# Performance work log

Measured on AMD Instinct MI355X. Metric: run time of the kernel, lower is better.

The kernel has to match this reference:

```python
import jax, jax.numpy as jnp
import numpy as np

EPSILON = 0.1
ALPHA = 0.5
N_ITER = 10
N_USERS = 100000


def setup_inputs() -> dict:
    key = jax.random.key(0)
    k1, k2, k3, k4, k5, k6 = jax.random.split(key, 6)
    B, C, F = 2048, 1024, 128
    users = jax.random.randint(k1, (B,), 0, N_USERS)
    items = jax.random.randint(k2, (B, C), 0, C)
    D = jax.random.uniform(k3, (B, C), minval=0.1, maxval=1.0)
    capacities = jax.random.uniform(k4, (C,), minval=0.5, maxval=1.5)
    # ScaledEmbedding: normal init scaled down by embedding_dim
    item_emb = jax.random.normal(k5, (C, F), dtype=jnp.float32) / F
    user_emb = jax.random.normal(k6, (N_USERS, F), dtype=jnp.float32) / F
    return dict(users=users, items=items, D=D, capacities=capacities,
                item_emb=item_emb, user_emb=user_emb)


def reference(users, items, D, capacities, item_emb, user_emb):
    B, C = D.shape
    ie = item_emb[items]            # [B, C, F] gathered candidate embeddings
    ue = user_emb[users]            # [B, F]
    dot = jnp.einsum('bcf,bf->bc', ie, ue)          # batched dot products
    affinity = (1.0 - ALPHA) * dot - ALPHA * (D / jnp.mean(D))
    K = jnp.exp(affinity / EPSILON)                 # [B, C]

    scaling = B / N_USERS
    a = jnp.ones((B,), K.dtype)
    b = capacities * scaling                        # [C]

    def step(carry, _):
        _, v = carry
        u = a / (K @ v)                             # [B]
        v_new = b / (K.T @ u)                       # [C]
        return (u, v_new), None

    (u, v), _ = jax.lax.scan(step, (a, jnp.ones((C,), K.dtype)),
                             None, length=N_ITER)
    P = K * (u[:, None] * v[None, :])               # K * outer(u, v)
    return P
```

## Files before the change

kernel.cpp:

```cpp
#include <hip/hip_runtime.h>
#include <hip/hip_fp16.h>

#define BB      2048
#define CC      1024
#define FF      128
#define NBLK    256
#define RPB     8
#define TPB     512
#define NITER   10
#define SUBR    8
#define SCALING_F (2048.0f / 100000.0f)

__device__ float g_K[BB * CC];
__device__ float g_meanPart[NBLK];
__device__ float g_colsum[NITER * SUBR * CC];

__global__ void __launch_bounds__(TPB)
k0_prep(const float* __restrict__ D) {
    const int bid = blockIdx.x, tid = threadIdx.x;
    for (int i = bid * TPB + tid; i < NITER * SUBR * CC; i += NBLK * TPB)
        g_colsum[i] = 0.0f;
    const float4* D4 = (const float4*)D;
    float p = 0.0f;
    for (int i = bid * TPB + tid; i < BB * CC / 4; i += NBLK * TPB) {
        float4 d = D4[i];
        p += d.x + d.y + d.z + d.w;
    }
    #pragma unroll
    for (int off = 32; off > 0; off >>= 1) p += __shfl_down(p, off, 64);
    __shared__ float red[TPB / 64];
    if ((tid & 63) == 0) red[tid >> 6] = p;
    __syncthreads();
    if (tid == 0) {
        float s = 0.0f;
        #pragma unroll
        for (int k = 0; k < TPB / 64; ++k) s += red[k];
        g_meanPart[bid] = s;
    }
}

__global__ void __launch_bounds__(TPB)
k1_buildK(const int* __restrict__ users, const int* __restrict__ items,
          const float* __restrict__ D, const float* __restrict__ iemb,
          const float* __restrict__ uemb) {
    const int bid = blockIdx.x, tid = threadIdx.x;
    const int r0 = bid * RPB;

    __shared__ float  uesh[RPB][FF];
    __shared__ __half dott[RPB][CC];
    __shared__ float  s2sh;

    if (tid < 256) {
        int r = tid >> 5, f4 = tid & 31;
        int u = users[r0 + r];
        ((float4*)uesh[r])[f4] = ((const float4*)(uemb + (size_t)u * FF))[f4];
    }
    if (tid < 64) {
        float s = g_meanPart[tid] + g_meanPart[tid + 64] +
                  g_meanPart[tid + 128] + g_meanPart[tid + 192];
        #pragma unroll
        for (int off = 32; off > 0; off >>= 1) s += __shfl_down(s, off, 64);
        if (tid == 0) s2sh = 5.0f * (float)(BB * CC) / s;
    }
    __syncthreads();

    const float4* us = (const float4*)uesh;
    #pragma unroll
    for (int jj = 0; jj < CC / TPB; ++jj) {
        int j = jj * TPB + tid;
        float acc[RPB] = {};
        const float4* ip = (const float4*)(iemb + (size_t)j * FF);
        for (int f4 = 0; f4 < FF / 4; ++f4) {
            float4 a = ip[f4];
            #pragma unroll
            for (int r = 0; r < RPB; ++r) {
                float4 b = us[r * (FF / 4) + f4];
                acc[r] += a.x * b.x + a.y * b.y + a.z * b.z + a.w * b.w;
            }
        }
        #pragma unroll
        for (int r = 0; r < RPB; ++r) dott[r][j] = __float2half(acc[r]);
    }
    __syncthreads();

    const float s2 = s2sh;
    const int4*   it4 = (const int4*)(items + ((size_t)r0 << 10));
    const float4* D4  = (const float4*)(D + ((size_t)r0 << 10));
    float4*       K4  = (float4*)(g_K + ((size_t)r0 << 10));
    for (int i = tid; i < RPB * CC / 4; i += TPB) {
        int4 iv = it4[i];
        float4 d = D4[i];
        int r = i >> 8;
        float4 kv;
        kv.x = __expf(5.0f * __half2float(dott[r][iv.x]) - s2 * d.x);
        kv.y = __expf(5.0f * __half2float(dott[r][iv.y]) - s2 * d.y);
        kv.z = __expf(5.0f * __half2float(dott[r][iv.z]) - s2 * d.z);
        kv.w = __expf(5.0f * __half2float(dott[r][iv.w]) - s2 * d.w);
        K4[i] = kv;
    }
}

__global__ void __launch_bounds__(TPB)
k_iter(const float* __restrict__ caps, int t) {
    const int bid = blockIdx.x, tid = threadIdx.x;
    const int r0 = bid * RPB;

    __shared__ float Kt[RPB][CC];
    __shared__ float vsh[CC];
    __shared__ float ush[RPB];

    for (int c = tid; c < CC; c += TPB) {
        float v = 1.0f;
        if (t > 0) {
            const float* base = g_colsum + (size_t)(t - 1) * SUBR * CC;
            float s = 0.0f;
            #pragma unroll
            for (int k = 0; k < SUBR; ++k) s += base[k * CC + c];
            v = caps[c] * SCALING_F / s;
        }
        vsh[c] = v;
    }
    const float4* Kg = (const float4*)(g_K + ((size_t)r0 << 10));
    float4* KtL = (float4*)Kt;
    for (int i = tid; i < RPB * CC / 4; i += TPB) KtL[i] = Kg[i];
    __syncthreads();

    {
        int r = tid >> 6, l = tid & 63;
        const float4* kr = (const float4*)Kt[r];
        const float4* v4 = (const float4*)vsh;
        float p = 0.0f;
        #pragma unroll
        for (int i = 0; i < 4; ++i) {
            float4 k = kr[l + i * 64], v = v4[l + i * 64];
            p += k.x * v.x + k.y * v.y + k.z * v.z + k.w * v.w;
        }
        #pragma unroll
        for (int off = 32; off > 0; off >>= 1) p += __shfl_down(p, off, 64);
        if (l == 0) ush[r] = 1.0f / p;
    }
    __syncthreads();

    float* cb = g_colsum + ((size_t)t * SUBR + (bid & (SUBR - 1))) * CC;
    for (int c = tid; c < CC; c += TPB) {
        float s = 0.0f;
        #pragma unroll
        for (int r = 0; r < RPB; ++r) s += Kt[r][c] * ush[r];
        atomicAdd(&cb[c], s);
    }
}

__global__ void __launch_bounds__(TPB)
k_final(const float* __restrict__ caps, float* __restrict__ out) {
    const int bid = blockIdx.x, tid = threadIdx.x;
    const int r0 = bid * RPB;

    __shared__ float Kt[RPB][CC];
    __shared__ float vsh[CC];
    __shared__ float ush[RPB];

    for (int c = tid; c < CC; c += TPB) {
        const float* base = g_colsum + (size_t)(NITER - 2) * SUBR * CC;
        float s = 0.0f;
        #pragma unroll
        for (int k = 0; k < SUBR; ++k) s += base[k * CC + c];
        vsh[c] = caps[c] * SCALING_F / s;
    }
    const float4* Kg = (const float4*)(g_K + ((size_t)r0 << 10));
    float4* KtL = (float4*)Kt;
    for (int i = tid; i < RPB * CC / 4; i += TPB) KtL[i] = Kg[i];
    __syncthreads();

    {
        int r = tid >> 6, l = tid & 63;
        const float4* kr = (const float4*)Kt[r];
        const float4* v4 = (const float4*)vsh;
        float p = 0.0f;
        #pragma unroll
        for (int i = 0; i < 4; ++i) {
            float4 k = kr[l + i * 64], v = v4[l + i * 64];
            p += k.x * v.x + k.y * v.y + k.z * v.z + k.w * v.w;
        }
        #pragma unroll
        for (int off = 32; off > 0; off >>= 1) p += __shfl_down(p, off, 64);
        if (l == 0) ush[r] = 1.0f / p;
    }
    __syncthreads();

    for (int c = tid; c < CC; c += TPB) {
        const float* base = g_colsum + (size_t)(NITER - 1) * SUBR * CC;
        float s = 0.0f;
        #pragma unroll
        for (int k = 0; k < SUBR; ++k) s += base[k * CC + c];
        vsh[c] = caps[c] * SCALING_F / s;
    }
    __syncthreads();

    float4* o4 = (float4*)(out + ((size_t)r0 << 10));
    for (int i = tid; i < RPB * CC / 4; i += TPB) {
        int r = i >> 8;
        float4 k = KtL[i];
        float  ur = ush[r];
        float4 v = *(const float4*)&vsh[(i * 4) & (CC - 1)];
        float4 p;
        p.x = k.x * ur * v.x;  p.y = k.y * ur * v.y;
        p.z = k.z * ur * v.z;  p.w = k.w * ur * v.w;
        o4[i] = p;
    }
}

extern "C" void kernel_launch(void* const* d_in, const int* in_sizes, int n_in,
                              void* d_out, int out_size, void* d_ws, size_t ws_size,
                              hipStream_t stream) {
    const int*   users = (const int*)d_in[0];
    const int*   items = (const int*)d_in[1];
    const float* D     = (const float*)d_in[2];
    const float* caps  = (const float*)d_in[3];
    const float* iemb  = (const float*)d_in[4];
    const float* uemb  = (const float*)d_in[5];
    float* out = (float*)d_out;

    hipLaunchKernelGGL(k0_prep,   dim3(NBLK), dim3(TPB), 0, stream, D);
    hipLaunchKernelGGL(k1_buildK, dim3(NBLK), dim3(TPB), 0, stream,
                       users, items, D, iemb, uemb);
    for (int t = 0; t < NITER; ++t)
        hipLaunchKernelGGL(k_iter, dim3(NBLK), dim3(TPB), 0, stream, caps, t);
    hipLaunchKernelGGL(k_final,  dim3(NBLK), dim3(TPB), 0, stream, caps, out);
}
```

Baseline: 192.6 us.

## Fuse all Sinkhorn stages into one cooperative persistent kernel with grid syncs

Replaces the thirteen separate launches (prep, K build, ten iterations, final) with one cooperative kernel that uses grid-wide syncs between phases. Each block keeps its 8-row K tile resident in shared memory for the whole run, so the global K buffer and its per-iteration reloads go away, and D is read only once. The costs removed are launch gaps and repeated 8 MB K traffic. In exchange the kernel depends on all 256 blocks being co-resident, uses more shared memory per block, and pays a grid barrier on every iteration.

```diff
diff --git a/kernel.cpp b/kernel.cpp
--- a/kernel.cpp
+++ b/kernel.cpp
@@ -1,5 +1,8 @@
 #include <hip/hip_runtime.h>
 #include <hip/hip_fp16.h>
+#include <hip/hip_cooperative_groups.h>
+
+namespace cg = cooperative_groups;
 
 #define BB      2048
 #define CC      1024
@@ -11,60 +14,55 @@
 #define SUBR    8
 #define SCALING_F (2048.0f / 100000.0f)
 
-__device__ float g_K[BB * CC];
 __device__ float g_meanPart[NBLK];
 __device__ float g_colsum[NITER * SUBR * CC];
 
 __global__ void __launch_bounds__(TPB)
-k0_prep(const float* __restrict__ D) {
+fused_sinkhorn(const int* __restrict__ users, const int* __restrict__ items,
+               const float* __restrict__ D, const float* __restrict__ caps,
+               const float* __restrict__ iemb, const float* __restrict__ uemb,
+               float* __restrict__ out) {
     const int bid = blockIdx.x, tid = threadIdx.x;
+    const int r0 = bid * RPB;
+
+    __shared__ union { float ue[RPB][FF]; float v[CC]; } uv;
+    __shared__ __half dott[RPB][CC];
+    __shared__ float  Kt[RPB][CC];
+    __shared__ float  ush[RPB];
+    __shared__ float  red[TPB / 64];
+    __shared__ float  s2sh;
+
     for (int i = bid * TPB + tid; i < NITER * SUBR * CC; i += NBLK * TPB)
-        g_colsum[i] = 0.0f;
-    const float4* D4 = (const float4*)D;
+        __hip_atomic_store(&g_colsum[i], 0.0f, __ATOMIC_RELAXED,
+                           __HIP_MEMORY_SCOPE_AGENT);
+
+    if (tid < 256) {
+        int r = tid >> 5, f4 = tid & 31;
+        int u = users[r0 + r];
+        ((float4*)uv.ue[r])[f4] = ((const float4*)(uemb + (size_t)u * FF))[f4];
+    }
+
+    const float4* Dg  = (const float4*)(D + ((size_t)r0 << 10));
+    float4*       KtL = (float4*)Kt;
     float p = 0.0f;
-    for (int i = bid * TPB + tid; i < BB * CC / 4; i += NBLK * TPB) {
-        float4 d = D4[i];
+    for (int i = tid; i < RPB * CC / 4; i += TPB) {
+        float4 d = Dg[i];
+        KtL[i] = d;
         p += d.x + d.y + d.z + d.w;
     }
     #pragma unroll
     for (int off = 32; off > 0; off >>= 1) p += __shfl_down(p, off, 64);
-    __shared__ float red[TPB / 64];
     if ((tid & 63) == 0) red[tid >> 6] = p;
     __syncthreads();
     if (tid == 0) {
         float s = 0.0f;
         #pragma unroll
         for (int k = 0; k < TPB / 64; ++k) s += red[k];
-        g_meanPart[bid] = s;
+        __hip_atomic_store(&g_meanPart[bid], s, __ATOMIC_RELAXED,
+                           __HIP_MEMORY_SCOPE_AGENT);
     }
-}
 
-__global__ void __launch_bounds__(TPB)
-k1_buildK(const int* __restrict__ users, const int* __restrict__ items,
-          const float* __restrict__ D, const float* __restrict__ iemb,
-          const float* __restrict__ uemb) {
-    const int bid = blockIdx.x, tid = threadIdx.x;
-    const int r0 = bid * RPB;
-
-    __shared__ float  uesh[RPB][FF];
-    __shared__ __half dott[RPB][CC];
-    __shared__ float  s2sh;
-
-    if (tid < 256) {
-        int r = tid >> 5, f4 = tid & 31;
-        int u = users[r0 + r];
-        ((float4*)uesh[r])[f4] = ((const float4*)(uemb + (size_t)u * FF))[f4];
-    }
-    if (tid < 64) {
-        float s = g_meanPart[tid] + g_meanPart[tid + 64] +
-                  g_meanPart[tid + 128] + g_meanPart[tid + 192];
-        #pragma unroll
-        for (int off = 32; off > 0; off >>= 1) s += __shfl_down(s, off, 64);
-        if (tid == 0) s2sh = 5.0f * (float)(BB * CC) / s;
-    }
-    __syncthreads();
-
-    const float4* us = (const float4*)uesh;
+    const float4* us = (const float4*)uv.ue;
     #pragma unroll
     for (int jj = 0; jj < CC / TPB; ++jj) {
         int j = jj * TPB + tid;
@@ -81,131 +79,100 @@
         #pragma unroll
         for (int r = 0; r < RPB; ++r) dott[r][j] = __float2half(acc[r]);
     }
+
+    cg::this_grid().sync();
+
+    if (tid < 64) {
+        float s = 0.0f;
+        #pragma unroll
+        for (int k = 0; k < NBLK / 64; ++k)
+            s += __hip_atomic_load(&g_meanPart[tid + 64 * k], __ATOMIC_RELAXED,
+                                   __HIP_MEMORY_SCOPE_AGENT);
+        #pragma unroll
+        for (int off = 32; off > 0; off >>= 1) s += __shfl_down(s, off, 64);
+        if (tid == 0) s2sh = 5.0f * (float)(BB * CC) / s;
+    }
     __syncthreads();
-
     const float s2 = s2sh;
-    const int4*   it4 = (const int4*)(items + ((size_t)r0 << 10));
-    const float4* D4  = (const float4*)(D + ((size_t)r0 << 10));
-    float4*       K4  = (float4*)(g_K + ((size_t)r0 << 10));
+    const int4* it4 = (const int4*)(items + ((size_t)r0 << 10));
     for (int i = tid; i < RPB * CC / 4; i += TPB) {
-        int4 iv = it4[i];
-        float4 d = D4[i];
-        int r = i >> 8;
+        int4   iv = it4[i];
+        float4 d  = KtL[i];
+        int    r  = i >> 8;
         float4 kv;
         kv.x = __expf(5.0f * __half2float(dott[r][iv.x]) - s2 * d.x);
         kv.y = __expf(5.0f * __half2float(dott[r][iv.y]) - s2 * d.y);
         kv.z = __expf(5.0f * __half2float(dott[r][iv.z]) - s2 * d.z);
         kv.w = __expf(5.0f * __half2float(dott[r][iv.w]) - s2 * d.w);
-        K4[i] = kv;
+        KtL[i] = kv;
     }
-}
 
-__global__ void __launch_bounds__(TPB)
-k_iter(const float* __restrict__ caps, int t) {
-    const int bid = blockIdx.x, tid = threadIdx.x;
-    const int r0 = bid * RPB;
+    for (int t = 0; t < NITER; ++t) {
+        if (t == 0) {
+            for (int c = tid; c < CC; c += TPB) uv.v[c] = 1.0f;
+        } else {
+            float* base = g_colsum + (size_t)(t - 1) * SUBR * CC;
+            for (int c = tid; c < CC; c += TPB) {
+                float s = 0.0f;
+                #pragma unroll
+                for (int k = 0; k < SUBR; ++k)
+                    s += __hip_atomic_load(&base[k * CC + c], __ATOMIC_RELAXED,
+                                           __HIP_MEMORY_SCOPE_AGENT);
+                uv.v[c] = caps[c] * SCALING_F / s;
+            }
+        }
+        __syncthreads();
 
-    __shared__ float Kt[RPB][CC];
-    __shared__ float vsh[CC];
-    __shared__ float ush[RPB];
+        {
+            int r = tid >> 6, l = tid & 63;
+            const float4* kr = (const float4*)Kt[r];
+            const float4* v4 = (const float4*)uv.v;
+            float pp = 0.0f;
+            #pragma unroll
+            for (int i2 = 0; i2 < 4; ++i2) {
+                float4 k = kr[l + i2 * 64], v = v4[l + i2 * 64];
+                pp += k.x * v.x + k.y * v.y + k.z * v.z + k.w * v.w;
+            }
+            #pragma unroll
+            for (int off = 32; off > 0; off >>= 1) pp += __shfl_down(pp, off, 64);
+            if (l == 0) ush[r] = 1.0f / pp;
+        }
+        __syncthreads();
 
-    for (int c = tid; c < CC; c += TPB) {
-        float v = 1.0f;
-        if (t > 0) {
-            const float* base = g_colsum + (size_t)(t - 1) * SUBR * CC;
+        float* cb = g_colsum + ((size_t)t * SUBR + (bid & (SUBR - 1))) * CC;
+        for (int c = tid; c < CC; c += TPB) {
             float s = 0.0f;
             #pragma unroll
-            for (int k = 0; k < SUBR; ++k) s += base[k * CC + c];
-            v = caps[c] * SCALING_F / s;
+            for (int r = 0; r < RPB; ++r) s += Kt[r][c] * ush[r];
+            atomicAdd(&cb[c], s);
         }
-        vsh[c] = v;
+
+        cg::this_grid().sync();
     }
-    const float4* Kg = (const float4*)(g_K + ((size_t)r0 << 10));
-    float4* KtL = (float4*)Kt;
-    for (int i = tid; i < RPB * CC / 4; i += TPB) KtL[i] = Kg[i];
-    __syncthreads();
 
     {
-        int r = tid >> 6, l = tid & 63;
-        const float4* kr = (const float4*)Kt[r];
-        const float4* v4 = (const float4*)vsh;
-        float p = 0.0f;
-        #pragma unroll
-        for (int i = 0; i < 4; ++i) {
-            float4 k = kr[l + i * 64], v = v4[l + i * 64];
-            p += k.x * v.x + k.y * v.y + k.z * v.z + k.w * v.w;
+        float* base = g_colsum + (size_t)(NITER - 1) * SUBR * CC;
+        for (int c = tid; c < CC; c += TPB) {
+            float s = 0.0f;
+            #pragma unroll
+            for (int k = 0; k < SUBR; ++k)
+                s += __hip_atomic_load(&base[k * CC + c], __ATOMIC_RELAXED,
+                                       __HIP_MEMORY_SCOPE_AGENT);
+            uv.v[c] = caps[c] * SCALING_F / s;
         }
-        #pragma unroll
-        for (int off = 32; off > 0; off >>= 1) p += __shfl_down(p, off, 64);
-        if (l == 0) ush[r] = 1.0f / p;
-    }
-    __syncthreads();
-
-    float* cb = g_colsum + ((size_t)t * SUBR + (bid & (SUBR - 1))) * CC;
-    for (int c = tid; c < CC; c += TPB) {
-        float s = 0.0f;
-        #pragma unroll
-        for (int r = 0; r < RPB; ++r) s += Kt[r][c] * ush[r];
-        atomicAdd(&cb[c], s);
-    }
-}
-
-__global__ void __launch_bounds__(TPB)
-k_final(const float* __restrict__ caps, float* __restrict__ out) {
-    const int bid = blockIdx.x, tid = threadIdx.x;
-    const int r0 = bid * RPB;
-
-    __shared__ float Kt[RPB][CC];
-    __shared__ float vsh[CC];
-    __shared__ float ush[RPB];
-
-    for (int c = tid; c < CC; c += TPB) {
-        const float* base = g_colsum + (size_t)(NITER - 2) * SUBR * CC;
-        float s = 0.0f;
-        #pragma unroll
-        for (int k = 0; k < SUBR; ++k) s += base[k * CC + c];
-        vsh[c] = caps[c] * SCALING_F / s;
-    }
-    const float4* Kg = (const float4*)(g_K + ((size_t)r0 << 10));
-    float4* KtL = (float4*)Kt;
-    for (int i = tid; i < RPB * CC / 4; i += TPB) KtL[i] = Kg[i];
-    __syncthreads();
-
-    {
-        int r = tid >> 6, l = tid & 63;
-        const float4* kr = (const float4*)Kt[r];
-        const float4* v4 = (const float4*)vsh;
-        float p = 0.0f;
-        #pragma unroll
-        for (int i = 0; i < 4; ++i) {
-            float4 k = kr[l + i * 64], v = v4[l + i * 64];
-            p += k.x * v.x + k.y * v.y + k.z * v.z + k.w * v.w;
-        }
-        #pragma unroll
-        for (int off = 32; off > 0; off >>= 1) p += __shfl_down(p, off, 64);
-        if (l == 0) ush[r] = 1.0f / p;
-    }
-    __syncthreads();
-
-    for (int c = tid; c < CC; c += TPB) {
-        const float* base = g_colsum + (size_t)(NITER - 1) * SUBR * CC;
-        float s = 0.0f;
-        #pragma unroll
-        for (int k = 0; k < SUBR; ++k) s += base[k * CC + c];
-        vsh[c] = caps[c] * SCALING_F / s;
     }
     __syncthreads();
 
     float4* o4 = (float4*)(out + ((size_t)r0 << 10));
     for (int i = tid; i < RPB * CC / 4; i += TPB) {
-        int r = i >> 8;
-        float4 k = KtL[i];
+        int    r  = i >> 8;
+        float4 k  = KtL[i];
         float  ur = ush[r];
-        float4 v = *(const float4*)&vsh[(i * 4) & (CC - 1)];
-        float4 p;
-        p.x = k.x * ur * v.x;  p.y = k.y * ur * v.y;
-        p.z = k.z * ur * v.z;  p.w = k.w * ur * v.w;
-        o4[i] = p;
+        float4 v  = *(const float4*)&uv.v[(i * 4) & (CC - 1)];
+        float4 pv;
+        pv.x = k.x * ur * v.x;  pv.y = k.y * ur * v.y;
+        pv.z = k.z * ur * v.z;  pv.w = k.w * ur * v.w;
+        o4[i] = pv;
     }
 }
 
@@ -220,10 +187,8 @@
     const float* uemb  = (const float*)d_in[5];
     float* out = (float*)d_out;
 
-    hipLaunchKernelGGL(k0_prep,   dim3(NBLK), dim3(TPB), 0, stream, D);
-    hipLaunchKernelGGL(k1_buildK, dim3(NBLK), dim3(TPB), 0, stream,
-                       users, items, D, iemb, uemb);
-    for (int t = 0; t < NITER; ++t)
-        hipLaunchKernelGGL(k_iter, dim3(NBLK), dim3(TPB), 0, stream, caps, t);
-    hipLaunchKernelGGL(k_final,  dim3(NBLK), dim3(TPB), 0, stream, caps, out);
+    void* args[] = { (void*)&users, (void*)&items, (void*)&D, (void*)&caps,
+                     (void*)&iemb, (void*)&uemb, (void*)&out };
+    hipLaunchCooperativeKernel((const void*)fused_sinkhorn,
+                               dim3(NBLK), dim3(TPB), args, 0, stream);
 }
```

Measured after the change: 421.0 us. 119% more time.
